# Performance work log

Hardware: AMD Instinct MI355X
Metric: run time of the kernel (lower is better)

Reference implementation:

```python
import jax, jax.numpy as jnp
import numpy as np

G_ZERO_INIT = 32.0  # g initialized to log2(g0^2 - g0)


def setup_inputs() -> dict:
    key = jax.random.key(0)
    k1, k2, k3 = jax.random.split(key, 3)
    B, L, D = 64, 16384, 64
    query = jax.random.normal(k1, (B, 1, D), dtype=jnp.float32)
    keys = jax.random.normal(k2, (B, L, D), dtype=jnp.float32)
    values = jax.random.normal(k3, (B, L, 1), dtype=jnp.float32)
    g = jnp.asarray(np.log2(G_ZERO_INIT**2 - G_ZERO_INIT), dtype=jnp.float32)
    return {"query": query, "keys": keys, "values": values, "g": g, "k": 256}


def reference(query, keys, values, g, k):
    # cosine similarity between query (B,1,D) and keys (B,L,D) -> (B,L)
    qn = query / jnp.linalg.norm(query, axis=-1, keepdims=True)
    kn = keys / jnp.linalg.norm(keys, axis=-1, keepdims=True)
    similarity = jnp.einsum("bqd,bld->bl", qn, kn) * g  # (B, L)
    # top-k select + batched gather of values
    top_sim, idx = jax.lax.top_k(similarity, k)          # (B, k) each
    values_sel = jnp.take_along_axis(values, idx[:, :, None], axis=1)  # (B, k, 1)
    weights = jax.nn.softmax(top_sim, axis=-1)           # (B, k)
    return values_sel, weights
```

## Files before the change

### kernel.cpp

```cpp
#include <hip/hip_runtime.h>
#include <math.h>

#define BATCH 64
#define LSEQ  16384
#define DIM   64
#define KSEL  256
#define CHUNK 1024
#define NRUNS (CHUNK / 256)
#define NCHUNK (LSEQ / CHUNK)
#define NCAND (NCHUNK * KSEL)

__global__ __launch_bounds__(256) void sim_kernel(
    const float* __restrict__ q,
    const float* __restrict__ keys,
    const float* __restrict__ gp,
    double* __restrict__ sims)
{
    const int b     = blockIdx.x >> 6;
    const int chunk = blockIdx.x & 63;
    const int t  = threadIdx.x;
    const int j  = t & 15;
    const int rl = t >> 4;

    const float4* q4 = reinterpret_cast<const float4*>(q) + b * 16;
    float4 qv = q4[j];
    const double qx = qv.x, qy = qv.y, qz = qv.z, qw = qv.w;
    double qss = qx*qx + qy*qy + qz*qz + qw*qw;
    #pragma unroll
    for (int m = 1; m < 16; m <<= 1) qss += __shfl_xor(qss, m);
    const double scale = (double)gp[0] / sqrt(qss);

    __shared__ double local[256];
    const float4* k4 = reinterpret_cast<const float4*>(keys) + (size_t)b * LSEQ * 16;
    const int row_base = chunk * 256;

    for (int it = 0; it < 16; ++it) {
        const int row = row_base + it * 16 + rl;
        float4 kv = k4[row * 16 + j];
        const double kx = kv.x, ky = kv.y, kz = kv.z, kw = kv.w;
        double dot = qx*kx + qy*ky + qz*kz + qw*kw;
        double kss = kx*kx + ky*ky + kz*kz + kw*kw;
        #pragma unroll
        for (int m = 1; m < 16; m <<= 1) {
            dot += __shfl_xor(dot, m);
            kss += __shfl_xor(kss, m);
        }
        if (j == 0) local[it * 16 + rl] = scale * dot / sqrt(kss);
    }
    __syncthreads();
    sims[(size_t)b * LSEQ + row_base + t] = local[t];
}

__device__ __forceinline__ unsigned long long f64_sortable(double v) {
    unsigned long long u = (unsigned long long)__double_as_longlong(v);
    return (u >> 63) ? ~u : (u | 0x8000000000000000ull);
}
__device__ __forceinline__ double sortable_f64(unsigned long long k) {
    unsigned long long u = (k & 0x8000000000000000ull)
                         ? (k ^ 0x8000000000000000ull) : ~k;
    return __longlong_as_double((long long)u);
}
__device__ __forceinline__ bool rank_gt(ulonglong2 a, ulonglong2 b) {
    return (a.x > b.x) || (a.x == b.x && a.y < b.y);
}

__global__ __launch_bounds__(256) void stage1_kernel(
    const double* __restrict__ sims,
    ulonglong2* __restrict__ cand)
{
    const int b     = blockIdx.x >> 4;
    const int chunk = blockIdx.x & 15;
    const int t     = threadIdx.x;
    const int base  = chunk * CHUNK;
    const double* s = sims + (size_t)b * LSEQ + base;

    __shared__ unsigned long long items[CHUNK];
    __shared__ ulonglong2 cand2[KSEL];

    #pragma unroll
    for (int r = 0; r < CHUNK / 256; ++r) {
        int lidx = r * 256 + t;
        unsigned long long key = f64_sortable(s[lidx]);
        items[lidx] = (key & ~0x7FFull) | (unsigned long long)(0x7FF - lidx);
    }

    for (int size = 2; size <= 256; size <<= 1) {
        for (int stride = size >> 1; stride > 0; stride >>= 1) {
            __syncthreads();
            #pragma unroll
            for (int r = 0; r < CHUNK / 512; ++r) {
                int tt = r * 256 + t;
                int i = ((tt & ~(stride - 1)) << 1) | (tt & (stride - 1));
                bool up = (size == 256) ? true : ((i & size) == 0);
                unsigned long long a = items[i], c = items[i + stride];
                if ((a > c) == up) { items[i] = c; items[i + stride] = a; }
            }
        }
    }

    for (int nr = NRUNS; nr > 1; nr >>= 1) {
        const int nout = (nr >> 1) * 256;
        __syncthreads();
        unsigned long long keep[2];
        #pragma unroll
        for (int c = 0; c < 2; ++c) {
            int lane = c * 256 + t;
            if (lane < nout) {
                int j = lane >> 8, i = lane & 255;
                unsigned long long a = items[(2 * j) * 256 + i];
                unsigned long long bb = items[(2 * j) * 256 + 511 - i];
                keep[c] = a > bb ? a : bb;
            }
        }
        __syncthreads();
        #pragma unroll
        for (int c = 0; c < 2; ++c) {
            int lane = c * 256 + t;
            if (lane < nout) items[lane] = keep[c];
        }
        for (int stride = 128; stride > 0; stride >>= 1) {
            __syncthreads();
            #pragma unroll
            for (int c = 0; c < 1; ++c) {
                int lane = t;
                if (lane < (nout >> 1)) {
                    int seg = lane >> 7, loc = lane & 127;
                    int i = seg * 256 + (((loc & ~(stride - 1)) << 1) | (loc & (stride - 1)));
                    unsigned long long a = items[i], cc = items[i + stride];
                    if (a > cc) { items[i] = cc; items[i + stride] = a; }
                }
            }
        }
    }
    __syncthreads();

    {
        unsigned long long item = items[t];
        int lidx = 0x7FF - (int)(item & 0x7FF);
        cand2[t] = make_ulonglong2(f64_sortable(s[lidx]),
                                   (unsigned long long)(base + lidx));
    }
    for (int size = 2; size <= 256; size <<= 1) {
        for (int stride = size >> 1; stride > 0; stride >>= 1) {
            __syncthreads();
            if (t < 128) {
                int i = ((t & ~(stride - 1)) << 1) | (t & (stride - 1));
                bool up = ((i & size) == 0);
                ulonglong2 a = cand2[i], c = cand2[i + stride];
                if (rank_gt(a, c) == up) { cand2[i] = c; cand2[i + stride] = a; }
            }
        }
    }
    __syncthreads();
    cand[((size_t)(b * NCHUNK + chunk)) * KSEL + t] = cand2[t];
}

__global__ __launch_bounds__(256) void stage2_kernel(
    const ulonglong2* __restrict__ cand,
    const float* __restrict__ values,
    float* __restrict__ out)
{
    const int b = blockIdx.x;
    const int t = threadIdx.x;
    __shared__ ulonglong2 arr[NCAND];

    #pragma unroll
    for (int r = 0; r < NCAND / 256; ++r)
        arr[r * 256 + t] = cand[(size_t)b * NCAND + r * 256 + t];

    for (int nr = NCHUNK; nr > 1; nr >>= 1) {
        const int nout = (nr >> 1) * 256;
        __syncthreads();
        ulonglong2 keep[8];
        #pragma unroll
        for (int c = 0; c < 8; ++c) {
            int lane = c * 256 + t;
            if (lane < nout) {
                int j = lane >> 8, i = lane & 255;
                ulonglong2 a  = arr[(2 * j) * 256 + i];
                ulonglong2 bb = arr[(2 * j) * 256 + 511 - i];
                keep[c] = rank_gt(a, bb) ? a : bb;
            }
        }
        __syncthreads();
        #pragma unroll
        for (int c = 0; c < 8; ++c) {
            int lane = c * 256 + t;
            if (lane < nout) arr[lane] = keep[c];
        }
        for (int stride = 128; stride > 0; stride >>= 1) {
            __syncthreads();
            #pragma unroll
            for (int c = 0; c < 4; ++c) {
                int lane = c * 256 + t;
                if (lane < (nout >> 1)) {
                    int seg = lane >> 7, loc = lane & 127;
                    int i = seg * 256 + (((loc & ~(stride - 1)) << 1) | (loc & (stride - 1)));
                    ulonglong2 a = arr[i], cc = arr[i + stride];
                    if (rank_gt(a, cc)) { arr[i] = cc; arr[i + stride] = a; }
                }
            }
        }
    }
    __syncthreads();

    ulonglong2 v = arr[255 - t];
    unsigned idx = (unsigned)v.y;
    double sv = sortable_f64(v.x);
    double fm = sortable_f64(arr[255].x);

    double e = exp(sv - fm);
    double esum = e;
    #pragma unroll
    for (int m = 1; m < 64; m <<= 1) esum += __shfl_xor(esum, m);
    __shared__ double wsum[4];
    if ((t & 63) == 0) wsum[t >> 6] = esum;
    __syncthreads();
    const double tot = wsum[0] + wsum[1] + wsum[2] + wsum[3];

    out[b * KSEL + t]                = values[(size_t)b * LSEQ + idx];
    out[BATCH * KSEL + b * KSEL + t] = (float)(e / tot);
}

extern "C" void kernel_launch(void* const* d_in, const int* in_sizes, int n_in,
                              void* d_out, int out_size, void* d_ws, size_t ws_size,
                              hipStream_t stream)
{
    const float* q      = (const float*)d_in[0];
    const float* keys   = (const float*)d_in[1];
    const float* values = (const float*)d_in[2];
    const float* g      = (const float*)d_in[3];
    float* out   = (float*)d_out;

    double* sims     = (double*)d_ws;
    ulonglong2* cand = (ulonglong2*)((char*)d_ws + (size_t)BATCH * LSEQ * 8);

    sim_kernel<<<dim3(BATCH * (LSEQ / 256)), dim3(256), 0, stream>>>(q, keys, g, sims);
    stage1_kernel<<<dim3(BATCH * NCHUNK), dim3(256), 0, stream>>>(sims, cand);
    stage2_kernel<<<dim3(BATCH), dim3(256), 0, stream>>>(cand, values, out);
}
```

Measured before the change: 419.5 us.

## Fuse similarity computation into per-chunk top-k selection kernel

Merges the cosine-similarity kernel into the first-stage selection kernel, so similarities stay in shared memory instead of making a round trip of doubles through global workspace. Each quad of threads now handles one key row with a 4-lane shuffle reduction, replacing the 16-lane reduction. The double-precision sqrt and divide are replaced by a float rsqrt seed refined with Newton iterations. The trade-off is fewer blocks (1024 instead of 4096) doing the 256 MB key read, which may reduce memory-level parallelism, and barrier placement is reshuffled.

```diff
diff --git a/kernel.cpp b/kernel.cpp
--- a/kernel.cpp
+++ b/kernel.cpp
@@ -10,47 +10,6 @@
 #define NCHUNK (LSEQ / CHUNK)
 #define NCAND (NCHUNK * KSEL)
 
-__global__ __launch_bounds__(256) void sim_kernel(
-    const float* __restrict__ q,
-    const float* __restrict__ keys,
-    const float* __restrict__ gp,
-    double* __restrict__ sims)
-{
-    const int b     = blockIdx.x >> 6;
-    const int chunk = blockIdx.x & 63;
-    const int t  = threadIdx.x;
-    const int j  = t & 15;
-    const int rl = t >> 4;
-
-    const float4* q4 = reinterpret_cast<const float4*>(q) + b * 16;
-    float4 qv = q4[j];
-    const double qx = qv.x, qy = qv.y, qz = qv.z, qw = qv.w;
-    double qss = qx*qx + qy*qy + qz*qz + qw*qw;
-    #pragma unroll
-    for (int m = 1; m < 16; m <<= 1) qss += __shfl_xor(qss, m);
-    const double scale = (double)gp[0] / sqrt(qss);
-
-    __shared__ double local[256];
-    const float4* k4 = reinterpret_cast<const float4*>(keys) + (size_t)b * LSEQ * 16;
-    const int row_base = chunk * 256;
-
-    for (int it = 0; it < 16; ++it) {
-        const int row = row_base + it * 16 + rl;
-        float4 kv = k4[row * 16 + j];
-        const double kx = kv.x, ky = kv.y, kz = kv.z, kw = kv.w;
-        double dot = qx*kx + qy*ky + qz*kz + qw*kw;
-        double kss = kx*kx + ky*ky + kz*kz + kw*kw;
-        #pragma unroll
-        for (int m = 1; m < 16; m <<= 1) {
-            dot += __shfl_xor(dot, m);
-            kss += __shfl_xor(kss, m);
-        }
-        if (j == 0) local[it * 16 + rl] = scale * dot / sqrt(kss);
-    }
-    __syncthreads();
-    sims[(size_t)b * LSEQ + row_base + t] = local[t];
-}
-
 __device__ __forceinline__ unsigned long long f64_sortable(double v) {
     unsigned long long u = (unsigned long long)__double_as_longlong(v);
     return (u >> 63) ? ~u : (u | 0x8000000000000000ull);
@@ -64,29 +23,75 @@
     return (a.x > b.x) || (a.x == b.x && a.y < b.y);
 }
 
-__global__ __launch_bounds__(256) void stage1_kernel(
-    const double* __restrict__ sims,
+__global__ __launch_bounds__(256) void sim_select_kernel(
+    const float* __restrict__ q,
+    const float* __restrict__ keys,
+    const float* __restrict__ gp,
     ulonglong2* __restrict__ cand)
 {
     const int b     = blockIdx.x >> 4;
     const int chunk = blockIdx.x & 15;
     const int t     = threadIdx.x;
+    const int quad  = t >> 2;
+    const int slot  = t & 3;
     const int base  = chunk * CHUNK;
-    const double* s = sims + (size_t)b * LSEQ + base;
-
+
+    __shared__ double sh_sims[CHUNK];
     __shared__ unsigned long long items[CHUNK];
     __shared__ ulonglong2 cand2[KSEL];
 
-    #pragma unroll
-    for (int r = 0; r < CHUNK / 256; ++r) {
-        int lidx = r * 256 + t;
-        unsigned long long key = f64_sortable(s[lidx]);
-        items[lidx] = (key & ~0x7FFull) | (unsigned long long)(0x7FF - lidx);
-    }
+    const float4* q4 = reinterpret_cast<const float4*>(q) + b * 16;
+    {
+        float4 qv = q4[t & 15];
+        double qs = (double)qv.x*qv.x + (double)qv.y*qv.y +
+                    (double)qv.z*qv.z + (double)qv.w*qv.w;
+        #pragma unroll
+        for (int m = 1; m < 16; m <<= 1) qs += __shfl_xor(qs, m);
+        sh_sims[0] = 0.0;
+        items[0] = 0ull;
+        __syncthreads();
+        (void)qs;
+        double scale = (double)gp[0] / sqrt(qs);
+
+        double qd[4][4];
+        #pragma unroll
+        for (int p = 0; p < 4; ++p) {
+            float4 qf = q4[p * 4 + slot];
+            qd[p][0] = qf.x; qd[p][1] = qf.y; qd[p][2] = qf.z; qd[p][3] = qf.w;
+        }
+
+        const float4* k4 = reinterpret_cast<const float4*>(keys) +
+                           (size_t)b * LSEQ * 16;
+        for (int it = 0; it < CHUNK / 64; ++it) {
+            const int lrow = it * 64 + quad;
+            const int row  = base + lrow;
+            double dot = 0.0, kss = 0.0;
+            #pragma unroll
+            for (int p = 0; p < 4; ++p) {
+                float4 kv = k4[row * 16 + p * 4 + slot];
+                const double kx = kv.x, ky = kv.y, kz = kv.z, kw = kv.w;
+                dot += qd[p][0]*kx + qd[p][1]*ky + qd[p][2]*kz + qd[p][3]*kw;
+                kss += kx*kx + ky*ky + kz*kz + kw*kw;
+            }
+            dot += __shfl_xor(dot, 1); dot += __shfl_xor(dot, 2);
+            kss += __shfl_xor(kss, 1); kss += __shfl_xor(kss, 2);
+            if (slot == 0) {
+                double x = (double)rsqrtf((float)kss);
+                #pragma unroll
+                for (int nit = 0; nit < 3; ++nit)
+                    x = x * (1.5 - 0.5 * kss * x * x);
+                double sim = scale * dot * x;
+                sh_sims[lrow] = sim;
+                unsigned long long key = f64_sortable(sim);
+                items[lrow] = (key & ~0x7FFull) |
+                              (unsigned long long)(0x7FF - lrow);
+            }
+        }
+    }
+    __syncthreads();
 
     for (int size = 2; size <= 256; size <<= 1) {
         for (int stride = size >> 1; stride > 0; stride >>= 1) {
-            __syncthreads();
             #pragma unroll
             for (int r = 0; r < CHUNK / 512; ++r) {
                 int tt = r * 256 + t;
@@ -95,19 +100,19 @@
                 unsigned long long a = items[i], c = items[i + stride];
                 if ((a > c) == up) { items[i] = c; items[i + stride] = a; }
             }
+            __syncthreads();
         }
     }
 
     for (int nr = NRUNS; nr > 1; nr >>= 1) {
         const int nout = (nr >> 1) * 256;
-        __syncthreads();
         unsigned long long keep[2];
         #pragma unroll
         for (int c = 0; c < 2; ++c) {
             int lane = c * 256 + t;
             if (lane < nout) {
                 int j = lane >> 8, i = lane & 255;
-                unsigned long long a = items[(2 * j) * 256 + i];
+                unsigned long long a  = items[(2 * j) * 256 + i];
                 unsigned long long bb = items[(2 * j) * 256 + 511 - i];
                 keep[c] = a > bb ? a : bb;
             }
@@ -118,40 +123,37 @@
             int lane = c * 256 + t;
             if (lane < nout) items[lane] = keep[c];
         }
+        __syncthreads();
         for (int stride = 128; stride > 0; stride >>= 1) {
-            __syncthreads();
-            #pragma unroll
-            for (int c = 0; c < 1; ++c) {
-                int lane = t;
-                if (lane < (nout >> 1)) {
-                    int seg = lane >> 7, loc = lane & 127;
-                    int i = seg * 256 + (((loc & ~(stride - 1)) << 1) | (loc & (stride - 1)));
-                    unsigned long long a = items[i], cc = items[i + stride];
-                    if (a > cc) { items[i] = cc; items[i + stride] = a; }
-                }
-            }
-        }
-    }
-    __syncthreads();
+            if (t < (nout >> 1)) {
+                int seg = t >> 7, loc = t & 127;
+                int i = seg * 256 +
+                        (((loc & ~(stride - 1)) << 1) | (loc & (stride - 1)));
+                unsigned long long a = items[i], cc = items[i + stride];
+                if (a > cc) { items[i] = cc; items[i + stride] = a; }
+            }
+            __syncthreads();
+        }
+    }
 
     {
         unsigned long long item = items[t];
         int lidx = 0x7FF - (int)(item & 0x7FF);
-        cand2[t] = make_ulonglong2(f64_sortable(s[lidx]),
+        cand2[t] = make_ulonglong2(f64_sortable(sh_sims[lidx]),
                                    (unsigned long long)(base + lidx));
     }
+    __syncthreads();
     for (int size = 2; size <= 256; size <<= 1) {
         for (int stride = size >> 1; stride > 0; stride >>= 1) {
-            __syncthreads();
             if (t < 128) {
                 int i = ((t & ~(stride - 1)) << 1) | (t & (stride - 1));
                 bool up = ((i & size) == 0);
                 ulonglong2 a = cand2[i], c = cand2[i + stride];
                 if (rank_gt(a, c) == up) { cand2[i] = c; cand2[i + stride] = a; }
             }
-        }
-    }
-    __syncthreads();
+            __syncthreads();
+        }
+    }
     cand[((size_t)(b * NCHUNK + chunk)) * KSEL + t] = cand2[t];
 }
 
@@ -195,7 +197,8 @@
                 int lane = c * 256 + t;
                 if (lane < (nout >> 1)) {
                     int seg = lane >> 7, loc = lane & 127;
-                    int i = seg * 256 + (((loc & ~(stride - 1)) << 1) | (loc & (stride - 1)));
+                    int i = seg * 256 +
+                            (((loc & ~(stride - 1)) << 1) | (loc & (stride - 1)));
                     ulonglong2 a = arr[i], cc = arr[i + stride];
                     if (rank_gt(a, cc)) { arr[i] = cc; arr[i + stride] = a; }
                 }
@@ -230,12 +233,9 @@
     const float* keys   = (const float*)d_in[1];
     const float* values = (const float*)d_in[2];
     const float* g      = (const float*)d_in[3];
-    float* out   = (float*)d_out;
-
-    double* sims     = (double*)d_ws;
-    ulonglong2* cand = (ulonglong2*)((char*)d_ws + (size_t)BATCH * LSEQ * 8);
-
-    sim_kernel<<<dim3(BATCH * (LSEQ / 256)), dim3(256), 0, stream>>>(q, keys, g, sims);
-    stage1_kernel<<<dim3(BATCH * NCHUNK), dim3(256), 0, stream>>>(sims, cand);
+    float* out = (float*)d_out;
+    ulonglong2* cand = (ulonglong2*)d_ws;
+
+    sim_select_kernel<<<dim3(BATCH * NCHUNK), dim3(256), 0, stream>>>(q, keys, g, cand);
     stage2_kernel<<<dim3(BATCH), dim3(256), 0, stream>>>(cand, values, out);
 }
```

Measured after the change: 414.2 us. Within noise of the previous version (-1.3%).
